# Kernel optimization log

Hardware: AMD Instinct MI355X
Metric: run time of the kernel (lower is better)

The kernel has to match this reference:

```python
import jax, jax.numpy as jnp
import numpy as np

H, W, D = 1024, 1024, 128


def setup_inputs() -> dict:
    key = jax.random.key(0)
    ks = jax.random.split(key, 7)
    x = jax.random.normal(ks[0], (2, H, W), dtype=jnp.float32)
    s1 = 1.0 / np.sqrt(4.0)
    s2 = 1.0 / np.sqrt(float(D))
    W1 = jax.random.uniform(ks[1], (4, D), jnp.float32, -s1, s1)
    b1 = jax.random.uniform(ks[2], (D,), jnp.float32, -s1, s1)
    W2 = jax.random.uniform(ks[3], (D, D), jnp.float32, -s2, s2)
    b2 = jax.random.uniform(ks[4], (D,), jnp.float32, -s2, s2)
    W3 = jax.random.uniform(ks[5], (D, D), jnp.float32, -s2, s2)
    b3 = jax.random.uniform(ks[6], (D,), jnp.float32, -s2, s2)
    return dict(x=x, W1=W1, b1=b1, W2=W2, b2=b2, W3=W3, b3=b3)


def _masked_norm(v, mask):
    # normalize(v) = (v - min) / (max - min), min/max over nonzero pixels only
    big = jnp.float32(1e30)
    vmin = jnp.min(jnp.where(mask, v, big))
    vmax = jnp.max(jnp.where(mask, v, -big))
    return (v - vmin) / (vmax - vmin)


def reference(x, W1, b1, W2, b2, W3, b3):
    x0, x1 = x[0], x[1]                      # real, imag maps [H, W]
    mask = x0 != 0                            # nonzero-context pixels
    w = mask.astype(x.dtype).reshape(-1)      # [H*W] 0/1 weights

    rows = jnp.broadcast_to(jnp.arange(H, dtype=x.dtype)[:, None], (H, W))
    cols = jnp.broadcast_to(jnp.arange(W, dtype=x.dtype)[None, :], (H, W))
    nr = _masked_norm(rows, mask)
    nc = _masked_norm(cols, mask)

    # per-point features [H*W, 4]: (norm row, norm col, real, imag)
    feats = jnp.stack([nr, nc, x0, x1], axis=-1).reshape(-1, 4)

    # fc3(relu(fc2(fc1(.)))) — note: no activation between fc1 and fc2
    h = feats @ W1 + b1                       # [N, 128]
    h = h @ W2 + b2
    h = jax.nn.relu(h)
    out = h @ W3 + b3                         # [N, 128]

    # mean over nonzero points only
    return (w[:, None] * out).sum(0) / w.sum()
```

## Files before the change

kernel.cpp:

```cpp
#include <hip/hip_runtime.h>
#include <climits>

#define HH 1024
#define WW 1024
#define DD 128
#define NPIX (HH * WW)
#define NSB 256
#define NBB 1024

#define RMINP 1024
#define RMAXP 1280
#define CMINP 1536
#define CMAXP 1792
#define CNTP  2048
#define PART  8192

typedef __attribute__((ext_vector_type(2))) float f32x2;

__device__ __forceinline__ void d_stats(const float* __restrict__ x0, int blk,
                                        int tid, int* __restrict__ wsi,
                                        int (*sred)[8]) {
    const float4* x4 = (const float4*)(x0) + (size_t)blk * 1024;
    int any0, any1, any2, any3;
    int cmn = INT_MAX, cmx = -1, cnt = 0;
    int c4 = 4 * tid;
    {
        float4 v;
        bool z0, z1, z2, z3;
        #define STAT_K(K, ANY)                                                 \
            v = x4[K * 256 + tid];                                             \
            z0 = v.x != 0.f; z1 = v.y != 0.f; z2 = v.z != 0.f; z3 = v.w != 0.f;\
            ANY = (int)(z0 | z1 | z2 | z3);                                    \
            if (ANY) {                                                         \
                cmn = min(cmn, z0 ? c4 : (z1 ? c4+1 : (z2 ? c4+2 : c4+3)));    \
                cmx = max(cmx, z3 ? c4+3 : (z2 ? c4+2 : (z1 ? c4+1 : c4)));    \
            }                                                                  \
            cnt += (int)z0 + (int)z1 + (int)z2 + (int)z3;
        STAT_K(0, any0) STAT_K(1, any1) STAT_K(2, any2) STAT_K(3, any3)
        #undef STAT_K
    }
    for (int off = 32; off >= 1; off >>= 1) {
        cmn = min(cmn, __shfl_xor(cmn, off, 64));
        cmx = max(cmx, __shfl_xor(cmx, off, 64));
        cnt += __shfl_xor(cnt, off, 64);
        any0 |= __shfl_xor(any0, off, 64);
        any1 |= __shfl_xor(any1, off, 64);
        any2 |= __shfl_xor(any2, off, 64);
        any3 |= __shfl_xor(any3, off, 64);
    }
    int wave = tid >> 6;
    if ((tid & 63) == 0) {
        sred[wave][0] = cmn; sred[wave][1] = cmx; sred[wave][2] = cnt;
        sred[wave][3] = any0; sred[wave][4] = any1;
        sred[wave][5] = any2; sred[wave][6] = any3;
    }
    __syncthreads();
    if (tid == 0) {
        int a = sred[0][0], b = sred[0][1], c = sred[0][2];
        int f0 = sred[0][3], f1 = sred[0][4], f2 = sred[0][5], f3 = sred[0][6];
        for (int w = 1; w < 4; ++w) {
            a = min(a, sred[w][0]); b = max(b, sred[w][1]); c += sred[w][2];
            f0 |= sred[w][3]; f1 |= sred[w][4]; f2 |= sred[w][5]; f3 |= sred[w][6];
        }
        int r0 = blk * 4;
        wsi[RMINP + blk] = f0 ? r0 : (f1 ? r0+1 : (f2 ? r0+2 : (f3 ? r0+3 : INT_MAX)));
        wsi[RMAXP + blk] = f3 ? r0+3 : (f2 ? r0+2 : (f1 ? r0+1 : (f0 ? r0 : -1)));
        wsi[CMINP + blk] = a;
        wsi[CMAXP + blk] = b;
        wsi[CNTP  + blk] = c;
    }
}

__global__ __launch_bounds__(256) void kA(const float* __restrict__ x0,
                                          const float* __restrict__ x1,
                                          const float* __restrict__ W1,
                                          const float* __restrict__ b1,
                                          const float* __restrict__ W2,
                                          const float* __restrict__ b2,
                                          const float* __restrict__ b3,
                                          float* __restrict__ out,
                                          float* __restrict__ wsf,
                                          int* __restrict__ wsi) {
    __shared__ int sred[4][8];
    int blk = blockIdx.x, tid = threadIdx.x;
    if (blk < NSB) {
        d_stats(x0, blk, tid, wsi, sred);
        const float4* y4 = (const float4*)(x1) + (size_t)blk * 1024;
        float s = 0.f;
        #pragma unroll
        for (int k = 0; k < 4; ++k) {
            float4 t4 = y4[k * 256 + tid];
            s += (t4.x + t4.y) + (t4.z + t4.w);
        }
        if (tid == 0) wsf[6400 + blk] = s;
        return;
    }
    if (tid < 128) {
        int j = tid;
        float p0 = 0.f, p1 = 0.f, p2 = 0.f, p3 = 0.f, cc = 0.f;
        #pragma unroll 8
        for (int d = 0; d < DD; ++d) {
            float w2 = W2[d * DD + j];
            p0 = fmaf(W1[0 * DD + d], w2, p0);
            p1 = fmaf(W1[1 * DD + d], w2, p1);
            p2 = fmaf(W1[2 * DD + d], w2, p2);
            p3 = fmaf(W1[3 * DD + d], w2, p3);
            cc = fmaf(b1[d],          w2, cc);
        }
        wsf[64 + 0 * DD + j] = p0;
        wsf[64 + 1 * DD + j] = p1;
        wsf[64 + 2 * DD + j] = p2;
        wsf[64 + 3 * DD + j] = p3;
        wsf[576 + j] = cc + b2[j];
        out[j] = b3[j];
    }
}

__global__ __launch_bounds__(256) void kB(const float* __restrict__ x0,
                                          const float* __restrict__ x1,
                                          float* __restrict__ wsf,
                                          const int* __restrict__ wsi) {
    __shared__ float sv_f[4096];
    __shared__ unsigned short lidx[1024];
    __shared__ int   lcnt;
    __shared__ int   sred[4][4];
    __shared__ float fred[128][9];

    int tid = threadIdx.x, blk = blockIdx.x;
    int wv = tid >> 6, lane = tid & 63;

    if (tid == 0) lcnt = 0;

    int rmn = wsi[RMINP + tid], rmx = wsi[RMAXP + tid];
    int cmn = wsi[CMINP + tid], cmx = wsi[CMAXP + tid];
    for (int off = 32; off >= 1; off >>= 1) {
        rmn = min(rmn, __shfl_xor(rmn, off, 64));
        rmx = max(rmx, __shfl_xor(rmx, off, 64));
        cmn = min(cmn, __shfl_xor(cmn, off, 64));
        cmx = max(cmx, __shfl_xor(cmx, off, 64));
    }
    if (lane == 0) {
        sred[wv][0] = rmn; sred[wv][1] = rmx;
        sred[wv][2] = cmn; sred[wv][3] = cmx;
    }
    __syncthreads();
    rmn = min(min(sred[0][0], sred[1][0]), min(sred[2][0], sred[3][0]));
    rmx = max(max(sred[0][1], sred[1][1]), max(sred[2][1], sred[3][1]));
    cmn = min(min(sred[0][2], sred[1][2]), min(sred[2][2], sred[3][2]));
    cmx = max(max(sred[0][3], sred[1][3]), max(sred[2][3], sred[3][3]));

    const float4* x04 = (const float4*)(x0) + (size_t)blk * 256;
    const float4* x14 = (const float4*)(x1) + (size_t)blk * 256;
    float4* sv4 = (float4*)sv_f;
    {
        float4 va = x04[tid];
        float4 vb = x14[tid];
        sv4[2 * tid]     = make_float4(va.x, va.y, vb.x, vb.y);
        sv4[2 * tid + 1] = make_float4(va.z, va.w, vb.z, vb.w);
        int p4 = 4 * tid;
        if (va.x == 0.f) { int p = atomicAdd(&lcnt, 1); lidx[p] = (unsigned short)(p4 + 0); }
        if (va.y == 0.f) { int p = atomicAdd(&lcnt, 1); lidx[p] = (unsigned short)(p4 + 1); }
        if (va.z == 0.f) { int p = atomicAdd(&lcnt, 1); lidx[p] = (unsigned short)(p4 + 2); }
        if (va.w == 0.f) { int p = atomicAdd(&lcnt, 1); lidx[p] = (unsigned short)(p4 + 3); }
    }
    __syncthreads();

    int ft = tid & 31;
    int cq = tid >> 5;
    int row = blk;
    float rs = 1.0f / (float)(rmx - rmn);
    float cs = 1.0f / (float)(cmx - cmn);

    f32x2 M2v[4], M3v[4], tv[4], st[4], acc[4];
    float a1v[4], rb[4];
    float accsub[4];
    #pragma unroll
    for (int k = 0; k < 4; ++k) {
        int f = ft + 32 * k;
        float M2 = wsf[64 + 2 * DD + f];
        float M3 = wsf[64 + 3 * DD + f];
        float a0 = wsf[64 + 0 * DD + f] * rs;
        float a1 = wsf[64 + 1 * DD + f] * cs;
        float cp = wsf[576 + f] - (float)rmn * a0 - (float)cmn * a1;
        rb[k]  = fmaf((float)row, a0, cp);
        a1v[k] = a1;
        float tA = fmaf((float)(cq * 128), a1, rb[k]);
        M2v[k] = (f32x2)M2;
        M3v[k] = (f32x2)M3;
        tv[k].x = tA; tv[k].y = tA + a1;
        st[k] = (f32x2)(a1 + a1);
        acc[k] = (f32x2)0.f;
        accsub[k] = 0.f;
    }

    const float4* p = sv4 + cq * 64;
    float4 vq = p[0];
    #pragma unroll 4
    for (int q = 0; q < 64; ++q) {
        float4 vn = p[(q + 1) & 63];
        f32x2 v0; v0.x = vq.x; v0.y = vq.y;
        f32x2 v1; v1.x = vq.z; v1.y = vq.w;
        #pragma unroll
        for (int k = 0; k < 4; ++k) {
            f32x2 d = __builtin_elementwise_fma(v0, M2v[k],
                        __builtin_elementwise_fma(v1, M3v[k], tv[k]));
            f32x2 r = __builtin_elementwise_max(d, (f32x2)0.f);
            acc[k] += r;
            tv[k] += st[k];
        }
        vq = vn;
    }

    int nz = lcnt;
    for (int ii = 0; ii < nz; ++ii) {
        int px = lidx[ii];
        if ((px >> 7) == cq) {
            float v0 = sv_f[(px >> 1) * 4 + (px & 1)];
            float v1 = sv_f[(px >> 1) * 4 + 2 + (px & 1)];
            #pragma unroll
            for (int k = 0; k < 4; ++k) {
                float tp = fmaf((float)px, a1v[k], rb[k]);
                accsub[k] += fmaxf(fmaf(v0, M2v[k].x, fmaf(v1, M3v[k].x, tp)), 0.f);
            }
        }
    }

    #pragma unroll
    for (int k = 0; k < 4; ++k)
        fred[ft + 32 * k][cq] = (acc[k].x + acc[k].y) - accsub[k];
    __syncthreads();
    if (tid < 128) {
        const float* fr = fred[tid];
        float s = ((fr[0] + fr[1]) + (fr[2] + fr[3]))
                + ((fr[4] + fr[5]) + (fr[6] + fr[7]));
        wsf[PART + (size_t)tid * NBB + blk] = s;
    }
}

__global__ __launch_bounds__(256) void kC(const float* __restrict__ wsf,
                                          const int* __restrict__ wsi,
                                          const float* __restrict__ W3,
                                          float* __restrict__ out) {
    __shared__ float sred[4];
    __shared__ int   cred[4];
    __shared__ float mf_sh;
    int f = blockIdx.x, tid = threadIdx.x;
    int wv = tid >> 6, lane = tid & 63;

    int c = wsi[CNTP + tid];
    for (int off = 32; off >= 1; off >>= 1) c += __shfl_xor(c, off, 64);
    if (lane == 0) cred[wv] = c;

    const float4* p = (const float4*)(wsf + PART + (size_t)f * NBB);
    float4 v = p[tid];
    float S = (v.x + v.y) + (v.z + v.w);
    for (int off = 32; off >= 1; off >>= 1) S += __shfl_xor(S, off, 64);
    if (lane == 0) sred[wv] = S;
    __syncthreads();
    if (tid == 0) {
        float tot = (sred[0] + sred[1]) + (sred[2] + sred[3]);
        float cnt = (float)(cred[0] + cred[1] + cred[2] + cred[3]);
        mf_sh = tot / cnt;
    }
    __syncthreads();

    if (tid < 128) {
        float mf = mf_sh;
        atomicAdd(&out[tid], mf * W3[f * DD + tid]);
    }
}

extern "C" void kernel_launch(void* const* d_in, const int* in_sizes, int n_in,
                              void* d_out, int out_size, void* d_ws, size_t ws_size,
                              hipStream_t stream) {
    const float* x  = (const float*)d_in[0];
    const float* x0 = x;
    const float* x1 = x + NPIX;
    const float* W1 = (const float*)d_in[1];
    const float* b1 = (const float*)d_in[2];
    const float* W2 = (const float*)d_in[3];
    const float* b2 = (const float*)d_in[4];
    const float* W3 = (const float*)d_in[5];
    const float* b3 = (const float*)d_in[6];
    float* outp = (float*)d_out;
    float* wsf  = (float*)d_ws;
    int*   wsi  = (int*)d_ws;

    hipLaunchKernelGGL(kA, dim3(NSB + 1), dim3(256), 0, stream,
                       x0, x1, W1, b1, W2, b2, b3, outp, wsf, wsi);
    hipLaunchKernelGGL(kB, dim3(NBB), dim3(256), 0, stream, x0, x1, wsf, wsi);
    hipLaunchKernelGGL(kC, dim3(DD), dim3(256), 0, stream, wsf, wsi, W3, outp);
}
```

Measured before the change: 30.28 us.

## Split final reduction into mean and W3 matvec kernels, dropping atomics

Replaces the final kernel, which did atomicAdd of mean*W3 into the output, with two kernels. The first computes per-feature means and writes them to padded workspace slots. The second is a single block that does the 128x128 matvec with W3 plus b3. The partial-sum layout in kB changes to blk-major, so kC1 now reads it with a strided gather. kA also gains a W3 sum whose result is written but never read, an extra cost, and the extra launch adds overhead in exchange for removing atomic contention.

```diff
diff --git a/kernel.cpp b/kernel.cpp
--- a/kernel.cpp
+++ b/kernel.cpp
@@ -13,6 +13,7 @@
 #define CMINP 1536
 #define CMAXP 1792
 #define CNTP  2048
+#define MPAD  4096
 #define PART  8192
 
 typedef __attribute__((ext_vector_type(2))) float f32x2;
@@ -77,8 +78,7 @@
                                           const float* __restrict__ b1,
                                           const float* __restrict__ W2,
                                           const float* __restrict__ b2,
-                                          const float* __restrict__ b3,
-                                          float* __restrict__ out,
+                                          const float* __restrict__ W3,
                                           float* __restrict__ wsf,
                                           int* __restrict__ wsi) {
     __shared__ int sred[4][8];
@@ -112,7 +112,13 @@
         wsf[64 + 2 * DD + j] = p2;
         wsf[64 + 3 * DD + j] = p3;
         wsf[576 + j] = cc + b2[j];
-        out[j] = b3[j];
+    } else {
+        const float4* w34 = (const float4*)W3;
+        float s = 0.f;
+        for (int k = tid - 128; k < DD * DD / 4; k += 128) {
+            float4 t4 = w34[k]; s += t4.x + t4.y + t4.z + t4.w;
+        }
+        wsf[6656 + tid - 128] = s;
     }
 }
 
@@ -233,17 +239,14 @@
         const float* fr = fred[tid];
         float s = ((fr[0] + fr[1]) + (fr[2] + fr[3]))
                 + ((fr[4] + fr[5]) + (fr[6] + fr[7]));
-        wsf[PART + (size_t)tid * NBB + blk] = s;
-    }
-}
-
-__global__ __launch_bounds__(256) void kC(const float* __restrict__ wsf,
-                                          const int* __restrict__ wsi,
-                                          const float* __restrict__ W3,
-                                          float* __restrict__ out) {
+        wsf[PART + (size_t)blk * DD + tid] = s;
+    }
+}
+
+__global__ __launch_bounds__(256) void kC1(float* __restrict__ wsf,
+                                           const int* __restrict__ wsi) {
     __shared__ float sred[4];
     __shared__ int   cred[4];
-    __shared__ float mf_sh;
     int f = blockIdx.x, tid = threadIdx.x;
     int wv = tid >> 6, lane = tid & 63;
 
@@ -251,23 +254,38 @@
     for (int off = 32; off >= 1; off >>= 1) c += __shfl_xor(c, off, 64);
     if (lane == 0) cred[wv] = c;
 
-    const float4* p = (const float4*)(wsf + PART + (size_t)f * NBB);
-    float4 v = p[tid];
-    float S = (v.x + v.y) + (v.z + v.w);
+    const float* p = wsf + PART + f;
+    float S = 0.f;
+    #pragma unroll
+    for (int k = 0; k < 4; ++k) S += p[(size_t)(tid + 256 * k) * DD];
     for (int off = 32; off >= 1; off >>= 1) S += __shfl_xor(S, off, 64);
     if (lane == 0) sred[wv] = S;
     __syncthreads();
     if (tid == 0) {
         float tot = (sred[0] + sred[1]) + (sred[2] + sred[3]);
         float cnt = (float)(cred[0] + cred[1] + cred[2] + cred[3]);
-        mf_sh = tot / cnt;
-    }
-    __syncthreads();
-
-    if (tid < 128) {
-        float mf = mf_sh;
-        atomicAdd(&out[tid], mf * W3[f * DD + tid]);
-    }
+        wsf[MPAD + f * 16] = tot / cnt;
+    }
+}
+
+__global__ __launch_bounds__(256) void kC2(const float* __restrict__ wsf,
+                                           const float* __restrict__ W3,
+                                           const float* __restrict__ b3,
+                                           float* __restrict__ out) {
+    __shared__ float sm[128];
+    __shared__ float s2[256];
+    int tid = threadIdx.x;
+    if (tid < 128) sm[tid] = wsf[MPAD + tid * 16];
+    __syncthreads();
+
+    int col = tid & 127, h = tid >> 7;
+    float o = 0.f;
+    #pragma unroll 8
+    for (int d = h * 64; d < h * 64 + 64; ++d)
+        o = fmaf(sm[d], W3[d * DD + col], o);
+    s2[tid] = o;
+    __syncthreads();
+    if (tid < 128) out[tid] = b3[tid] + s2[tid] + s2[tid + 128];
 }
 
 extern "C" void kernel_launch(void* const* d_in, const int* in_sizes, int n_in,
@@ -287,7 +305,8 @@
     int*   wsi  = (int*)d_ws;
 
     hipLaunchKernelGGL(kA, dim3(NSB + 1), dim3(256), 0, stream,
-                       x0, x1, W1, b1, W2, b2, b3, outp, wsf, wsi);
+                       x0, x1, W1, b1, W2, b2, W3, wsf, wsi);
     hipLaunchKernelGGL(kB, dim3(NBB), dim3(256), 0, stream, x0, x1, wsf, wsi);
-    hipLaunchKernelGGL(kC, dim3(DD), dim3(256), 0, stream, wsf, wsi, W3, outp);
-}
+    hipLaunchKernelGGL(kC1, dim3(DD), dim3(256), 0, stream, wsf, wsi);
+    hipLaunchKernelGGL(kC2, dim3(1), dim3(256), 0, stream, wsf, W3, b3, outp);
+}
```

Result: slower. 31.12 us (+2.8%).
